# Kernel tuning notes

Hardware: AMD Instinct MI355X
Metric: run time of the kernel (lower is better)

The kernel has to match this reference:

```python
import jax, jax.numpy as jnp
import numpy as np

N, E, D = 50000, 600000, 128
NEG_SLOPE = 0.2

def setup_inputs() -> dict:
    key = jax.random.key(0)
    ks = jax.random.split(key, 12)
    s = 1.0 / np.sqrt(D)
    return {
        "x": jax.random.normal(ks[0], (N, D), jnp.float32),
        "edge_index": jax.random.randint(ks[1], (2, E), 0, N),
        "edge_attr": jax.random.normal(ks[2], (E, D), jnp.float32),
        "ln1_g": jnp.ones((D,), jnp.float32),
        "ln1_b": jnp.zeros((D,), jnp.float32),
        "W_lin": jax.random.normal(ks[3], (D, D), jnp.float32) * s,
        "att_src": jax.random.normal(ks[4], (D,), jnp.float32) * s,
        "att_dst": jax.random.normal(ks[5], (D,), jnp.float32) * s,
        "W_edge": jax.random.normal(ks[6], (D, D), jnp.float32) * s,
        "att_edge": jax.random.normal(ks[7], (D,), jnp.float32) * s,
        "gat_bias": jnp.zeros((D,), jnp.float32),
        "ln2_g": jnp.ones((D,), jnp.float32),
        "ln2_b": jnp.zeros((D,), jnp.float32),
        "W1": jax.random.normal(ks[8], (D, 4 * D), jnp.float32) * s,
        "b1": jnp.zeros((4 * D,), jnp.float32),
        "W2": jax.random.normal(ks[9], (4 * D, D), jnp.float32) * (1.0 / np.sqrt(4 * D)),
        "b2": jnp.zeros((D,), jnp.float32),
    }


def _layernorm(x, g, b, eps=1e-5):
    mu = jnp.mean(x, axis=-1, keepdims=True)
    var = jnp.mean(jnp.square(x - mu), axis=-1, keepdims=True)
    return (x - mu) * jax.lax.rsqrt(var + eps) * g + b


def _gat_conv(x, edge_index, edge_attr, W_lin, att_src, att_dst, W_edge, att_edge, gat_bias):
    # PyG GATConv, heads=1, concat=False, add_self_loops=False, edge_dim=D
    src, dst = edge_index[0], edge_index[1]
    h = x @ W_lin                      # [N, D] shared src/dst projection
    a_src = h @ att_src                # [N]
    a_dst = h @ att_dst                # [N]
    a_edge = (edge_attr @ W_edge) @ att_edge  # [E]
    alpha = a_src[src] + a_dst[dst] + a_edge  # [E]
    alpha = jnp.where(alpha > 0, alpha, NEG_SLOPE * alpha)  # leaky_relu(0.2)
    # segment softmax over destination nodes
    m = jax.ops.segment_max(alpha, dst, num_segments=N)
    m = jnp.where(jnp.isfinite(m), m, 0.0)
    ex = jnp.exp(alpha - m[dst])
    denom = jax.ops.segment_sum(ex, dst, num_segments=N)
    coef = ex / jnp.maximum(denom[dst], 1e-16)
    # weighted scatter-aggregation of source messages
    out = jax.ops.segment_sum(coef[:, None] * h[src], dst, num_segments=N)
    return out + gat_bias


def reference(x, edge_index, edge_attr, ln1_g, ln1_b, W_lin, att_src, att_dst,
              W_edge, att_edge, gat_bias, ln2_g, ln2_b, W1, b1, W2, b2):
    # pre-norm + GAT message passing + residual (dropout = eval identity)
    xn = _layernorm(x, ln1_g, ln1_b)
    x = x + _gat_conv(xn, edge_index, edge_attr, W_lin, att_src, att_dst,
                      W_edge, att_edge, gat_bias)
    # pre-norm + FFN + residual
    xn = _layernorm(x, ln2_g, ln2_b)
    ffn = jax.nn.relu(xn @ W1 + b1) @ W2 + b2
    return x + ffn
```

## Files before the change

kernel.cpp:

```cpp
#include <hip/hip_runtime.h>

#define D 128
#define NEG_SLOPE 0.2f

typedef __attribute__((ext_vector_type(8))) short short8;
typedef __attribute__((ext_vector_type(4))) float f32x4;

__device__ __forceinline__ float wred_sum(float v){
#pragma unroll
  for (int m = 32; m; m >>= 1) v += __shfl_xor(v, m);
  return v;
}
__device__ __forceinline__ int wred_sumi(int v){
#pragma unroll
  for (int m = 32; m; m >>= 1) v += __shfl_xor(v, m);
  return v;
}
__device__ __forceinline__ float wred_max(float v){
#pragma unroll
  for (int m = 32; m; m >>= 1) v = fmaxf(v, __shfl_xor(v, m));
  return v;
}
__device__ __forceinline__ unsigned short bf16r(float f){
  unsigned int u = __float_as_uint(f);
  u += 0x7fffu + ((u >> 16) & 1u);
  return (unsigned short)(u >> 16);
}
__device__ __forceinline__ float bf2f(unsigned int hi16){
  return __uint_as_float(hi16 << 16);
}

__global__ void k_prep0(const float* __restrict__ W_lin, const float* __restrict__ W1,
                        const float* __restrict__ W2, const float* __restrict__ W_edge,
                        const float* __restrict__ att_edge,
                        unsigned short* __restrict__ Wlt, unsigned short* __restrict__ W1t,
                        unsigned short* __restrict__ W2t, float* __restrict__ we,
                        int* __restrict__ cnt, int N){
  int t = blockIdx.x * blockDim.x + threadIdx.x;
  if (t < N) cnt[t] = 0;
  if (t < 128 * 128){
    int c = t >> 7, k = t & 127;
    Wlt[t] = bf16r(W_lin[k * 128 + c]);
  } else if (t < 128 * 128 + 512 * 128){
    int u = t - 128 * 128; int c = u >> 7, k = u & 127;
    W1t[u] = bf16r(W1[k * 512 + c]);
  } else if (t < 128 * 128 + 512 * 128 + 128 * 512){
    int u = t - (128 * 128 + 512 * 128); int c = u >> 9, k = u & 511;
    W2t[u] = bf16r(W2[k * 128 + c]);
  } else {
    int u = t - (128 * 128 + 512 * 128 + 128 * 512);
    if (u < 128){
      float s = 0.f;
      for (int j = 0; j < 128; ++j) s += W_edge[u * 128 + j] * att_edge[j];
      we[u] = s;
    }
  }
}

__global__ __launch_bounds__(256) void k_hgemm(const float* __restrict__ x,
                                               const unsigned short* __restrict__ Wlt,
                                               const float* __restrict__ ln1_g,
                                               const float* __restrict__ ln1_b,
                                               const float* __restrict__ att_src,
                                               const float* __restrict__ att_dst,
                                               const int* __restrict__ ei,
                                               unsigned short* __restrict__ hq,
                                               float* __restrict__ asrc,
                                               float* __restrict__ adst,
                                               int* __restrict__ cnt, int N, int E){
  __shared__ unsigned short wbuf[16384];
#pragma unroll
  for (int r = 0; r < 8; ++r){
    int idx = r * 256 + threadIdx.x;
    int c = idx >> 4, kc = idx & 15;
    short8 w = *(const short8*)(Wlt + c * 128 + kc * 8);
    *(short8*)((char*)wbuf + c * 256 + ((kc * 16) ^ ((c & 7) << 4))) = w;
  }
  __syncthreads();
  int wid = threadIdx.x >> 6, lane = threadIdx.x & 63;
  int rb = blockIdx.x * 64 + wid * 16;
  int row = rb + (lane & 15);
  int rowc = row < N ? row : N - 1;
  int ksub = (lane >> 4) * 8;
  float v[4][8];
#pragma unroll
  for (int kb = 0; kb < 4; ++kb){
    float4 p0 = *(const float4*)(x + (size_t)rowc * 128 + kb * 32 + ksub);
    float4 p1 = *(const float4*)(x + (size_t)rowc * 128 + kb * 32 + ksub + 4);
    v[kb][0]=p0.x; v[kb][1]=p0.y; v[kb][2]=p0.z; v[kb][3]=p0.w;
    v[kb][4]=p1.x; v[kb][5]=p1.y; v[kb][6]=p1.z; v[kb][7]=p1.w;
  }
  float s = 0.f;
#pragma unroll
  for (int kb = 0; kb < 4; ++kb)
#pragma unroll
    for (int j = 0; j < 8; ++j) s += v[kb][j];
  s += __shfl_xor(s, 16); s += __shfl_xor(s, 32);
  float mu = s * (1.0f / 128.f);
  float q = 0.f;
#pragma unroll
  for (int kb = 0; kb < 4; ++kb)
#pragma unroll
    for (int j = 0; j < 8; ++j){ float d = v[kb][j] - mu; q += d * d; }
  q += __shfl_xor(q, 16); q += __shfl_xor(q, 32);
  float rstd = rsqrtf(q * (1.0f / 128.f) + 1e-5f);
  short8 a[4];
#pragma unroll
  for (int kb = 0; kb < 4; ++kb){
    float4 g0 = *(const float4*)(ln1_g + kb * 32 + ksub);
    float4 g1 = *(const float4*)(ln1_g + kb * 32 + ksub + 4);
    float4 b0 = *(const float4*)(ln1_b + kb * 32 + ksub);
    float4 b1 = *(const float4*)(ln1_b + kb * 32 + ksub + 4);
    float gg[8] = {g0.x,g0.y,g0.z,g0.w,g1.x,g1.y,g1.z,g1.w};
    float bb[8] = {b0.x,b0.y,b0.z,b0.w,b1.x,b1.y,b1.z,b1.w};
#pragma unroll
    for (int j = 0; j < 8; ++j)
      a[kb][j] = (short)bf16r((v[kb][j] - mu) * rstd * gg[j] + bb[j]);
  }
  f32x4 acc[8];
#pragma unroll
  for (int ct = 0; ct < 8; ++ct) acc[ct] = (f32x4){0.f, 0.f, 0.f, 0.f};
#pragma unroll
  for (int ct = 0; ct < 8; ++ct){
    int col = ct * 16 + (lane & 15);
    int cswz = (col & 7) << 4;
#pragma unroll
    for (int kb = 0; kb < 4; ++kb){
      short8 bf = *(const short8*)((const char*)wbuf + col * 256 +
                                   ((kb * 64 + ksub * 2) ^ cswz));
      acc[ct] = __builtin_amdgcn_mfma_f32_16x16x32_bf16(a[kb], bf, acc[ct], 0, 0, 0);
    }
  }
  int r0 = rb + (lane >> 4) * 4;
#pragma unroll
  for (int ct = 0; ct < 8; ++ct){
    int col = ct * 16 + (lane & 15);
#pragma unroll
    for (int j = 0; j < 4; ++j){
      int r = r0 + j;
      if (r < N) hq[(size_t)r * 128 + col] = bf16r(acc[ct][j]);
    }
  }
  float as_v[8], ad_v[8];
#pragma unroll
  for (int ct = 0; ct < 8; ++ct){
    int col = ct * 16 + (lane & 15);
    as_v[ct] = att_src[col];
    ad_v[ct] = att_dst[col];
  }
  float ps[4] = {0.f,0.f,0.f,0.f}, pd[4] = {0.f,0.f,0.f,0.f};
#pragma unroll
  for (int ct = 0; ct < 8; ++ct)
#pragma unroll
    for (int j = 0; j < 4; ++j){
      ps[j] += acc[ct][j] * as_v[ct];
      pd[j] += acc[ct][j] * ad_v[ct];
    }
#pragma unroll
  for (int m = 1; m < 16; m <<= 1)
#pragma unroll
    for (int j = 0; j < 4; ++j){
      ps[j] += __shfl_xor(ps[j], m);
      pd[j] += __shfl_xor(pd[j], m);
    }
  if ((lane & 15) == 0){
#pragma unroll
    for (int j = 0; j < 4; ++j){
      int r = r0 + j;
      if (r < N){ asrc[r] = ps[j]; adst[r] = pd[j]; }
    }
  }
  int t = blockIdx.x * blockDim.x + threadIdx.x;
  int stride = gridDim.x * blockDim.x;
  for (int e = t; e < E; e += stride) atomicAdd(&cnt[ei[E + e]], 1);
}

__global__ void k_escan(const int* __restrict__ cnt, int* __restrict__ start,
                        int* __restrict__ cursor, int N){
  int b = blockIdx.x, t = threadIdx.x;
  int base = b * 256;
  int acc = 0;
  for (int i = t; i < base; i += 256) acc += cnt[i];
  acc = wred_sumi(acc);
  __shared__ int wsum[4];
  if ((t & 63) == 0) wsum[t >> 6] = acc;
  __syncthreads();
  int s_off = wsum[0] + wsum[1] + wsum[2] + wsum[3];
  int i = base + t;
  int c = (i < N) ? cnt[i] : 0;
  __shared__ int sd[256];
  sd[t] = c;
  __syncthreads();
  for (int off = 1; off < 256; off <<= 1){
    int vv = (t >= off) ? sd[t - off] : 0;
    __syncthreads();
    sd[t] += vv;
    __syncthreads();
  }
  int st = s_off + sd[t] - c;
  if (i <= N) start[i] = st;
  if (i < N) cursor[i] = st;
}

__global__ void k_edge_scatter(const float* __restrict__ ea, const int* __restrict__ ei,
                               const float* __restrict__ we, const float* __restrict__ asrc,
                               const float* __restrict__ adst, int* __restrict__ cursor,
                               int2* __restrict__ esa, int E){
  int gw = (blockIdx.x * blockDim.x + threadIdx.x) >> 6;
  int lane = threadIdx.x & 63;
  int e = gw * 2 + (lane >> 5);
  int li = lane & 31;
  if (e >= E) return;
  float4 v = *(const float4*)(ea + (size_t)e * 128 + li * 4);
  float4 w = *(const float4*)(we + li * 4);
  float s = v.x * w.x + v.y * w.y + v.z * w.z + v.w * w.w;
#pragma unroll
  for (int m = 16; m; m >>= 1) s += __shfl_xor(s, m);
  if (li == 0){
    int sn = ei[e], dn = ei[E + e];
    float al = asrc[sn] + adst[dn] + s;
    al = al > 0.f ? al : NEG_SLOPE * al;
    int slot = atomicAdd(&cursor[dn], 1);
    esa[slot] = make_int2(sn, __float_as_int(al));
  }
}

__global__ void k_agg(const float* __restrict__ x, const unsigned short* __restrict__ hq,
                      const int* __restrict__ start, const int2* __restrict__ esa,
                      const float* __restrict__ gat_bias,
                      const float* __restrict__ g2, const float* __restrict__ b2,
                      float* __restrict__ out, unsigned short* __restrict__ xn2q, int N){
  int n = (blockIdx.x * blockDim.x + threadIdx.x) >> 6;
  int lane = threadIdx.x & 63;
  if (n >= N) return;
  int beg = start[n], end = start[n + 1];
  float m = -1e30f;
  for (int i = beg + lane; i < end; i += 64) m = fmaxf(m, __int_as_float(esa[i].y));
  m = wred_max(m);
  float ds = 0.f, a0 = 0.f, a1 = 0.f;
#pragma unroll 2
  for (int s = beg; s < end; ++s){
    int2 ev = esa[s];
    float ex = __expf(__int_as_float(ev.y) - m);
    ds += ex;
    unsigned int hv = *(const unsigned int*)(hq + (size_t)ev.x * 128 + lane * 2);
    a0 += ex * bf2f(hv & 0xffffu);
    a1 += ex * bf2f(hv >> 16);
  }
  float inv = (end > beg) ? 1.f / fmaxf(ds, 1e-16f) : 0.f;
  a0 *= inv; a1 *= inv;
  float2 xv  = *(const float2*)(x + (size_t)n * 128 + lane * 2);
  float2 gbv = *(const float2*)(gat_bias + lane * 2);
  float r0 = xv.x + a0 + gbv.x;
  float r1 = xv.y + a1 + gbv.y;
  float mu = wred_sum(r0 + r1) * (1.0f / 128.f);
  float d0 = r0 - mu, d1 = r1 - mu;
  float var = wred_sum(d0 * d0 + d1 * d1) * (1.0f / 128.f);
  float rstd = rsqrtf(var + 1e-5f);
  float2 gv = *(const float2*)(g2 + lane * 2);
  float2 bv = *(const float2*)(b2 + lane * 2);
  float o0 = d0 * rstd * gv.x + bv.x;
  float o1 = d1 * rstd * gv.y + bv.y;
  *(float2*)(out + (size_t)n * 128 + lane * 2) = make_float2(r0, r1);
  unsigned int pk = (unsigned int)bf16r(o0) | ((unsigned int)bf16r(o1) << 16);
  *(unsigned int*)(xn2q + (size_t)n * 128 + lane * 2) = pk;
}

__global__ __launch_bounds__(512) void k_ffn(const unsigned short* __restrict__ xn2q,
                                             const unsigned short* __restrict__ W1t,
                                             const unsigned short* __restrict__ W2t,
                                             const float* __restrict__ b1,
                                             const float* __restrict__ b2,
                                             float* __restrict__ out, int N, int T){
  __shared__ unsigned short w1lds[128 * 128];
  __shared__ unsigned short w2lds[128 * 128];
  __shared__ unsigned short hid[64 * 128];
  int tid = threadIdx.x;
  int wid = tid >> 6, lane = tid & 63;
  int rg = wid >> 1, ch = wid & 1;
  int i = lane & 15, g = lane >> 4;
  int t0 = blockIdx.x, t1 = blockIdx.x + gridDim.x;
  short8 a[2][4];
#pragma unroll
  for (int u = 0; u < 2; ++u){
    int t = u ? t1 : t0;
    if (t < T){
      int arow = t * 64 + rg * 16 + i;
      int arowc = arow < N ? arow : N - 1;
#pragma unroll
      for (int kb = 0; kb < 4; ++kb)
        a[u][kb] = *(const short8*)(xn2q + (size_t)arowc * 128 + kb * 32 + g * 8);
    }
  }
  f32x4 acc[2][4];
#pragma unroll
  for (int u = 0; u < 2; ++u)
#pragma unroll
    for (int ct = 0; ct < 4; ++ct) acc[u][ct] = (f32x4){0.f, 0.f, 0.f, 0.f};
#pragma unroll 1
  for (int c = 0; c < 4; ++c){
#pragma unroll
    for (int qq = 0; qq < 4; ++qq){
      int idx = qq * 512 + tid;
      int cl = idx >> 4, kc = idx & 15;
      int dst = cl * 256 + ((kc * 16) ^ ((cl & 7) << 4));
      short8 w1v = *(const short8*)(W1t + (size_t)(c * 128 + cl) * 128 + kc * 8);
      *(short8*)((char*)w1lds + dst) = w1v;
      short8 w2v = *(const short8*)(W2t + (size_t)cl * 512 + c * 128 + kc * 8);
      *(short8*)((char*)w2lds + dst) = w2v;
    }
    __syncthreads();
#pragma unroll 1
    for (int u = 0; u < 2; ++u){
      int t = u ? t1 : t0;
      if (t >= T) break;
#pragma unroll
      for (int ct = 0; ct < 4; ++ct){
        int hcol = ch * 64 + ct * 16 + i;
        int cswz = (hcol & 7) << 4;
        f32x4 hacc = {0.f, 0.f, 0.f, 0.f};
#pragma unroll
        for (int kb = 0; kb < 4; ++kb){
          short8 bf = *(const short8*)((const char*)w1lds + hcol * 256 +
                                       ((kb * 64 + g * 16) ^ cswz));
          hacc = __builtin_amdgcn_mfma_f32_16x16x32_bf16(a[u][kb], bf, hacc, 0, 0, 0);
        }
        float bias = b1[c * 128 + hcol];
#pragma unroll
        for (int j = 0; j < 4; ++j){
          float v = hacc[j] + bias;
          v = v > 0.f ? v : 0.f;
          int nl = rg * 16 + g * 4 + j;
          *(unsigned short*)((char*)hid + nl * 256 + ((hcol * 2) ^ ((nl & 7) << 4))) = bf16r(v);
        }
      }
      __syncthreads();
#pragma unroll
      for (int kbl = 0; kbl < 4; ++kbl){
        int nrow = rg * 16 + i;
        short8 af = *(const short8*)((const char*)hid + nrow * 256 +
                                     ((kbl * 64 + g * 16) ^ ((nrow & 7) << 4)));
#pragma unroll
        for (int ct = 0; ct < 4; ++ct){
          int ocol = ch * 64 + ct * 16 + i;
          short8 bf = *(const short8*)((const char*)w2lds + ocol * 256 +
                                       ((kbl * 64 + g * 16) ^ ((ocol & 7) << 4)));
          acc[u][ct] = __builtin_amdgcn_mfma_f32_16x16x32_bf16(af, bf, acc[u][ct], 0, 0, 0);
        }
      }
      __syncthreads();
    }
  }
#pragma unroll
  for (int u = 0; u < 2; ++u){
    int t = u ? t1 : t0;
    if (t >= T) break;
#pragma unroll
    for (int ct = 0; ct < 4; ++ct){
      int ocol = ch * 64 + ct * 16 + i;
      float bias = b2[ocol];
#pragma unroll
      for (int j = 0; j < 4; ++j){
        int row = t * 64 + rg * 16 + g * 4 + j;
        if (row < N) out[(size_t)row * 128 + ocol] += acc[u][ct][j] + bias;
      }
    }
  }
}

extern "C" void kernel_launch(void* const* d_in, const int* in_sizes, int n_in,
                              void* d_out, int out_size, void* d_ws, size_t ws_size,
                              hipStream_t stream){
  const float* x        = (const float*)d_in[0];
  const int*   ei       = (const int*)  d_in[1];
  const float* ea       = (const float*)d_in[2];
  const float* ln1_g    = (const float*)d_in[3];
  const float* ln1_b    = (const float*)d_in[4];
  const float* W_lin    = (const float*)d_in[5];
  const float* att_src  = (const float*)d_in[6];
  const float* att_dst  = (const float*)d_in[7];
  const float* W_edge   = (const float*)d_in[8];
  const float* att_edge = (const float*)d_in[9];
  const float* gat_bias = (const float*)d_in[10];
  const float* ln2_g    = (const float*)d_in[11];
  const float* ln2_b    = (const float*)d_in[12];
  const float* W1       = (const float*)d_in[13];
  const float* b1       = (const float*)d_in[14];
  const float* W2       = (const float*)d_in[15];
  const float* b2       = (const float*)d_in[16];

  const int N = in_sizes[0] / 128;
  const int E = in_sizes[2] / 128;
  const int T = (N + 63) / 64;
  float* out = (float*)d_out;

  char* pp = (char*)d_ws;
  auto carve = [&](size_t bytes) -> char* {
    char* r = pp; pp += (bytes + 255) & ~(size_t)255; return r;
  };
  unsigned short* hq     = (unsigned short*)carve((size_t)N * 128 * 2);
  unsigned short* xn2q   = (unsigned short*)carve((size_t)N * 128 * 2);
  float*          asrc   = (float*)carve((size_t)N * 4);
  float*          adst   = (float*)carve((size_t)N * 4);
  int2*           esa    = (int2*)carve((size_t)E * 8);
  int*            cnt    = (int*)carve((size_t)N * 4);
  int*            cursor = (int*)carve((size_t)N * 4);
  int*            start  = (int*)carve((size_t)(N + 1) * 4);
  unsigned short* Wlt    = (unsigned short*)carve(128 * 128 * 2);
  unsigned short* W1t    = (unsigned short*)carve(512 * 128 * 2);
  unsigned short* W2t    = (unsigned short*)carve(128 * 512 * 2);
  float*          we     = (float*)carve(128 * 4);

  k_prep0<<<(128*128 + 512*128 + 128*512 + 128 + 255) / 256, 256, 0, stream>>>(
      W_lin, W1, W2, W_edge, att_edge, Wlt, W1t, W2t, we, cnt, N);
  k_hgemm<<<(N + 63) / 64, 256, 0, stream>>>(x, Wlt, ln1_g, ln1_b, att_src, att_dst, ei,
                                             hq, asrc, adst, cnt, N, E);
  k_escan<<<N / 256 + 1, 256, 0, stream>>>(cnt, start, cursor, N);
  k_edge_scatter<<<(E + 7) / 8, 256, 0, stream>>>(ea, ei, we, asrc, adst, cursor, esa, E);
  k_agg<<<(N + 3) / 4, 256, 0, stream>>>(x, hq, start, esa, gat_bias, ln2_g, ln2_b,
                                         out, xn2q, N);
  k_ffn<<<512, 512, 0, stream>>>(xn2q, W1t, W2t, b1, b2, out, N, T);
}
```

Measured before the change: 331.3 us.

## Split FFN hidden dimension across blocks with resident weights and atomic accumulation

Each FFN block now owns one of four 128-wide hidden chunks and loads its W1/W2 slice into LDS once. It then loops over 32-row tiles, so weights are no longer reloaded per chunk per tile. Partial outputs from the four chunks are combined into the output with float atomicAdd, and b2 is added only by chunk 0. This trades weight reload traffic for four-way atomic contention on every output element, and the summation order becomes nondeterministic.

```diff
diff --git a/kernel.cpp b/kernel.cpp
--- a/kernel.cpp
+++ b/kernel.cpp
@@ -274,97 +274,83 @@
                                              float* __restrict__ out, int N, int T){
   __shared__ unsigned short w1lds[128 * 128];
   __shared__ unsigned short w2lds[128 * 128];
-  __shared__ unsigned short hid[64 * 128];
-  int tid = threadIdx.x;
-  int wid = tid >> 6, lane = tid & 63;
-  int rg = wid >> 1, ch = wid & 1;
-  int i = lane & 15, g = lane >> 4;
-  int t0 = blockIdx.x, t1 = blockIdx.x + gridDim.x;
-  short8 a[2][4];
-#pragma unroll
-  for (int u = 0; u < 2; ++u){
-    int t = u ? t1 : t0;
-    if (t < T){
-      int arow = t * 64 + rg * 16 + i;
-      int arowc = arow < N ? arow : N - 1;
-#pragma unroll
-      for (int kb = 0; kb < 4; ++kb)
-        a[u][kb] = *(const short8*)(xn2q + (size_t)arowc * 128 + kb * 32 + g * 8);
-    }
-  }
-  f32x4 acc[2][4];
-#pragma unroll
-  for (int u = 0; u < 2; ++u)
-#pragma unroll
-    for (int ct = 0; ct < 4; ++ct) acc[u][ct] = (f32x4){0.f, 0.f, 0.f, 0.f};
-#pragma unroll 1
-  for (int c = 0; c < 4; ++c){
-#pragma unroll
-    for (int qq = 0; qq < 4; ++qq){
-      int idx = qq * 512 + tid;
-      int cl = idx >> 4, kc = idx & 15;
-      int dst = cl * 256 + ((kc * 16) ^ ((cl & 7) << 4));
-      short8 w1v = *(const short8*)(W1t + (size_t)(c * 128 + cl) * 128 + kc * 8);
+  __shared__ unsigned short xnt[32 * 128];
+  __shared__ unsigned short hidt[32 * 128];
+  const int tid = threadIdx.x;
+  const int chunk = blockIdx.x & 3;
+  const int tb0 = blockIdx.x >> 2;
+#pragma unroll
+  for (int r = 0; r < 8; ++r){
+    int idx = r * 512 + tid;
+    int cl = (idx >> 4) & 127, kc = idx & 15;
+    int dst = cl * 256 + ((kc * 16) ^ ((cl & 7) << 4));
+    if (idx < 2048){
+      short8 w1v = *(const short8*)(W1t + (size_t)(chunk * 128 + cl) * 128 + kc * 8);
       *(short8*)((char*)w1lds + dst) = w1v;
-      short8 w2v = *(const short8*)(W2t + (size_t)cl * 512 + c * 128 + kc * 8);
+    } else {
+      short8 w2v = *(const short8*)(W2t + (size_t)cl * 512 + chunk * 128 + kc * 8);
       *(short8*)((char*)w2lds + dst) = w2v;
     }
+  }
+  const int wid = tid >> 6, lane = tid & 63;
+  const int i = lane & 15, g = lane >> 4;
+  const int rw = wid >> 2;
+  const int ca = wid & 3;
+  for (int t = tb0; t < T; t += 128){
+    {
+      int row = tid >> 4, kc = tid & 15;
+      int trow = t * 32 + row;
+      int trc = trow < N ? trow : N - 1;
+      short8 xv = *(const short8*)(xn2q + (size_t)trc * 128 + kc * 8);
+      *(short8*)((char*)xnt + row * 256 + ((kc * 16) ^ ((row & 7) << 4))) = xv;
+    }
     __syncthreads();
-#pragma unroll 1
-    for (int u = 0; u < 2; ++u){
-      int t = u ? t1 : t0;
-      if (t >= T) break;
-#pragma unroll
-      for (int ct = 0; ct < 4; ++ct){
-        int hcol = ch * 64 + ct * 16 + i;
-        int cswz = (hcol & 7) << 4;
-        f32x4 hacc = {0.f, 0.f, 0.f, 0.f};
-#pragma unroll
-        for (int kb = 0; kb < 4; ++kb){
-          short8 bf = *(const short8*)((const char*)w1lds + hcol * 256 +
-                                       ((kb * 64 + g * 16) ^ cswz));
-          hacc = __builtin_amdgcn_mfma_f32_16x16x32_bf16(a[u][kb], bf, hacc, 0, 0, 0);
-        }
-        float bias = b1[c * 128 + hcol];
-#pragma unroll
-        for (int j = 0; j < 4; ++j){
-          float v = hacc[j] + bias;
-          v = v > 0.f ? v : 0.f;
-          int nl = rg * 16 + g * 4 + j;
-          *(unsigned short*)((char*)hid + nl * 256 + ((hcol * 2) ^ ((nl & 7) << 4))) = bf16r(v);
-        }
+#pragma unroll
+    for (int ct = 0; ct < 2; ++ct){
+      int hcol = ca * 32 + ct * 16 + i;
+      int cswz = (hcol & 7) << 4;
+      f32x4 hacc = {0.f, 0.f, 0.f, 0.f};
+#pragma unroll
+      for (int kb = 0; kb < 4; ++kb){
+        int arow = rw * 16 + i;
+        short8 af = *(const short8*)((const char*)xnt + arow * 256 +
+                                     ((kb * 64 + g * 16) ^ ((arow & 7) << 4)));
+        short8 bf = *(const short8*)((const char*)w1lds + hcol * 256 +
+                                     ((kb * 64 + g * 16) ^ cswz));
+        hacc = __builtin_amdgcn_mfma_f32_16x16x32_bf16(af, bf, hacc, 0, 0, 0);
       }
-      __syncthreads();
+      float bias = b1[chunk * 128 + hcol];
+#pragma unroll
+      for (int j = 0; j < 4; ++j){
+        float v = hacc[j] + bias;
+        v = v > 0.f ? v : 0.f;
+        int nl = rw * 16 + g * 4 + j;
+        *(unsigned short*)((char*)hidt + nl * 256 + ((hcol * 2) ^ ((nl & 7) << 4))) = bf16r(v);
+      }
+    }
+    __syncthreads();
+#pragma unroll
+    for (int ct = 0; ct < 2; ++ct){
+      int ocol = ca * 32 + ct * 16 + i;
+      int cswz = (ocol & 7) << 4;
+      f32x4 oacc = {0.f, 0.f, 0.f, 0.f};
 #pragma unroll
       for (int kbl = 0; kbl < 4; ++kbl){
-        int nrow = rg * 16 + i;
-        short8 af = *(const short8*)((const char*)hid + nrow * 256 +
+        int nrow = rw * 16 + i;
+        short8 af = *(const short8*)((const char*)hidt + nrow * 256 +
                                      ((kbl * 64 + g * 16) ^ ((nrow & 7) << 4)));
-#pragma unroll
-        for (int ct = 0; ct < 4; ++ct){
-          int ocol = ch * 64 + ct * 16 + i;
-          short8 bf = *(const short8*)((const char*)w2lds + ocol * 256 +
-                                       ((kbl * 64 + g * 16) ^ ((ocol & 7) << 4)));
-          acc[u][ct] = __builtin_amdgcn_mfma_f32_16x16x32_bf16(af, bf, acc[u][ct], 0, 0, 0);
-        }
+        short8 bf = *(const short8*)((const char*)w2lds + ocol * 256 +
+                                     ((kbl * 64 + g * 16) ^ cswz));
+        oacc = __builtin_amdgcn_mfma_f32_16x16x32_bf16(af, bf, oacc, 0, 0, 0);
       }
-      __syncthreads();
-    }
-  }
-#pragma unroll
-  for (int u = 0; u < 2; ++u){
-    int t = u ? t1 : t0;
-    if (t >= T) break;
-#pragma unroll
-    for (int ct = 0; ct < 4; ++ct){
-      int ocol = ch * 64 + ct * 16 + i;
-      float bias = b2[ocol];
+      float bias = (chunk == 0) ? b2[ocol] : 0.f;
 #pragma unroll
       for (int j = 0; j < 4; ++j){
-        int row = t * 64 + rg * 16 + g * 4 + j;
-        if (row < N) out[(size_t)row * 128 + ocol] += acc[u][ct][j] + bias;
+        int row = t * 32 + rw * 16 + g * 4 + j;
+        if (row < N) atomicAdd(&out[(size_t)row * 128 + ocol], oacc[j] + bias);
       }
     }
+    __syncthreads();
   }
 }
 
@@ -391,7 +377,7 @@
 
   const int N = in_sizes[0] / 128;
   const int E = in_sizes[2] / 128;
-  const int T = (N + 63) / 64;
+  const int T32 = (N + 31) / 32;
   float* out = (float*)d_out;
 
   char* pp = (char*)d_ws;
@@ -419,5 +405,5 @@
   k_edge_scatter<<<(E + 7) / 8, 256, 0, stream>>>(ea, ei, we, asrc, adst, cursor, esa, E);
   k_agg<<<(N + 3) / 4, 256, 0, stream>>>(x, hq, start, esa, gat_bias, ln2_g, ln2_b,
                                          out, xn2q, N);
-  k_ffn<<<512, 512, 0, stream>>>(xn2q, W1t, W2t, b1, b2, out, N, T);
-}
+  k_ffn<<<512, 512, 0, stream>>>(xn2q, W1t, W2t, b1, b2, out, N, T32);
+}
```

Result: faster. 309.2 us (-6.7%).
